# Kernel tuning notes

Hardware: AMD Instinct MI355X
Metric: run time of the kernel (lower is better)

The kernel has to match this reference:

```python
import jax, jax.numpy as jnp
import numpy as np

B, C, H, W = 8, 512, 64, 64
D = C // 8        # attention feature dim for q/k
HID = 100         # pooling hidden dim


def setup_inputs() -> dict:
    key = jax.random.key(0)
    ks = jax.random.split(key, 12)
    s = 0.02
    return {
        "x": jax.random.normal(ks[0], (B, C, H, W), dtype=jnp.float32),
        "Wq": jax.random.normal(ks[1], (D, C), dtype=jnp.float32) * s,
        "bq": jnp.zeros((D,), dtype=jnp.float32),
        "Wk": jax.random.normal(ks[2], (D, C), dtype=jnp.float32) * s,
        "bk": jnp.zeros((D,), dtype=jnp.float32),
        "Wv": jax.random.normal(ks[3], (C, C), dtype=jnp.float32) * s,
        "bv": jnp.zeros((C,), dtype=jnp.float32),
        "gamma": jnp.zeros((1,), dtype=jnp.float32),
        "Wa": jax.random.normal(ks[4], (HID, C), dtype=jnp.float32) * s,
        "ba": jnp.zeros((HID,), dtype=jnp.float32),
        "Wc": jax.random.normal(ks[5], (1, HID), dtype=jnp.float32) * s,
    }


def reference(x, Wq, bq, Wk, bk, Wv, bv, gamma, Wa, ba, Wc):
    b, c, h, w = x.shape
    n = h * w
    xf = x.reshape(b, c, n)  # [B, C, N]

    # 1x1 convs == per-pixel channel matmuls
    q = jnp.einsum('dc,bcn->bdn', Wq, xf) + bq[None, :, None]  # [B, D, N]
    k = jnp.einsum('dc,bcn->bdn', Wk, xf) + bk[None, :, None]  # [B, D, N]
    v = jnp.einsum('ec,bcn->ben', Wv, xf) + bv[None, :, None]  # [B, C, N]

    # energy[b,i,j] = <q_i, k_j>; softmax over j (last dim)
    energy = jnp.einsum('bdi,bdj->bij', q, k)                  # [B, N, N]
    attn = jax.nn.softmax(energy, axis=-1)
    # out[b,c,i] = sum_j v[b,c,j] * attn[b,i,j]
    sa_out = jnp.einsum('bcj,bij->bci', v, attn)               # [B, C, N]
    hfeat = gamma[0] * sa_out + xf                             # [B, C, N]

    # attention pooling: linear -> tanh -> linear -> softmax over spatial
    a = jnp.tanh(jnp.einsum('hc,bcn->bnh', Wa, hfeat) + ba)    # [B, N, HID]
    score = jnp.einsum('oh,bnh->bn', Wc, a)                    # [B, N]
    amap = jax.nn.softmax(score, axis=1)                       # [B, N]

    # weighted sum of ORIGINAL input features (as in the torch code)
    return jnp.einsum('bcn,bn->bc', xf, amap)                  # [B, C]
```

## Files before the change

### kernel.cpp

```cpp
#include <hip/hip_runtime.h>
#include <hip/hip_bf16.h>

#define B_ 8
#define C_ 512
#define N_ 4096
#define D_ 64
#define HID_ 100
#define LDK 40

typedef short bf16x8 __attribute__((ext_vector_type(8)));
typedef short bf16x4 __attribute__((ext_vector_type(4)));
typedef float f32x4 __attribute__((ext_vector_type(4)));

__device__ __forceinline__ short f2bf(float f) {
  unsigned u = __builtin_bit_cast(unsigned, f);
  u += 0x7fff + ((u >> 16) & 1);
  return (short)(u >> 16);
}

__device__ __forceinline__ float fast_tanh(float x) {
  float cx = fminf(fmaxf(x, -15.f), 15.f);
  float a = exp2f(cx * 2.885390082f);
  return (a - 1.f) * __builtin_amdgcn_rcpf(a + 1.f);
}


__global__ __launch_bounds__(256) void qkv_proj(
    const float* __restrict__ x,
    const float* __restrict__ Wq, const float* __restrict__ bq,
    const float* __restrict__ Wk, const float* __restrict__ bk,
    const float* __restrict__ Wv, const float* __restrict__ bv,
    const float* __restrict__ gamma,
    float* __restrict__ q, float* __restrict__ k, float* __restrict__ v) {
  if (gamma[0] == 0.0f) return;
  const int ROWS = D_ + D_ + C_;
  const int TILES = N_ / 256;
  const int NJOBS = B_ * ROWS * TILES;
  for (int job = blockIdx.x; job < NJOBS; job += gridDim.x) {
    int tile = job % TILES;
    int row  = (job / TILES) % ROWS;
    int b    = job / (TILES * ROWS);
    int n = tile * 256 + threadIdx.x;
    const float* W;
    float bias;
    float* dst;
    if (row < D_) {
      W = Wq + (size_t)row * C_; bias = bq[row];
      dst = q + ((size_t)b * D_ + row) * N_;
    } else if (row < 2 * D_) {
      int r = row - D_;
      W = Wk + (size_t)r * C_; bias = bk[r];
      dst = k + ((size_t)b * D_ + r) * N_;
    } else {
      int r = row - 2 * D_;
      W = Wv + (size_t)r * C_; bias = bv[r];
      dst = v + ((size_t)b * C_ + r) * N_;
    }
    const float* xb = x + (size_t)b * C_ * N_ + n;
    float s = 0.f;
    for (int c = 0; c < C_; ++c) s += W[c] * xb[(size_t)c * N_];
    dst[n] = s + bias;
  }
}

__global__ __launch_bounds__(256) void attn_sa(
    const float* __restrict__ q, const float* __restrict__ k,
    const float* __restrict__ v, const float* __restrict__ gamma,
    float* __restrict__ sa) {
  if (gamma[0] == 0.0f) return;
  __shared__ float e[N_];
  __shared__ float qi[D_];
  __shared__ float red4[4];
  const int tid = threadIdx.x;
  for (int job = blockIdx.x; job < B_ * N_; job += gridDim.x) {
    int b = job >> 12;
    int i = job & (N_ - 1);
    if (tid < D_) qi[tid] = q[((size_t)b * D_ + tid) * N_ + i];
    __syncthreads();
    for (int j = tid; j < N_; j += 256) {
      float s = 0.f;
      for (int d = 0; d < D_; ++d) s += qi[d] * k[((size_t)b * D_ + d) * N_ + j];
      e[j] = s;
    }
    __syncthreads();
    float m = -1e30f;
    for (int j = tid; j < N_; j += 256) m = fmaxf(m, e[j]);
#pragma unroll
    for (int off = 32; off; off >>= 1) m = fmaxf(m, __shfl_xor(m, off));
    if ((tid & 63) == 0) red4[tid >> 6] = m;
    __syncthreads();
    float M = fmaxf(fmaxf(red4[0], red4[1]), fmaxf(red4[2], red4[3]));
    __syncthreads();
    float ssum = 0.f;
    for (int j = tid; j < N_; j += 256) {
      float p = expf(e[j] - M);
      e[j] = p;
      ssum += p;
    }
#pragma unroll
    for (int off = 32; off; off >>= 1) ssum += __shfl_xor(ssum, off);
    if ((tid & 63) == 0) red4[tid >> 6] = ssum;
    __syncthreads();
    float inv = 1.0f / (red4[0] + red4[1] + red4[2] + red4[3]);
    __syncthreads();
    for (int c = tid; c < C_; c += 256) {
      const float* vr = v + ((size_t)b * C_ + c) * N_;
      float s = 0.f;
      for (int j = 0; j < N_; ++j) s += vr[j] * e[j];
      sa[((size_t)b * C_ + c) * N_ + i] = s * inv;
    }
    __syncthreads();
  }
}

__global__ __launch_bounds__(256) void wa_to_bf16(
    const float* __restrict__ Wa, short* __restrict__ wab) {
  int flat = (blockIdx.x * 256 + threadIdx.x) * 4;
  int h = flat >> 9, c = flat & 511;
  bf16x4 p = {0, 0, 0, 0};
  if (h < HID_) {
    float4 w4 = *(const float4*)&Wa[(size_t)h * C_ + c];
    p = (bf16x4){f2bf(w4.x), f2bf(w4.y), f2bf(w4.z), f2bf(w4.w)};
  }
  *(bf16x4*)&wab[flat] = p;
}


__global__ __launch_bounds__(512, 2) void pool_gemm(
    const float* __restrict__ x, const float* __restrict__ sa,
    const float* __restrict__ gamma,
    const short* __restrict__ wab, const float* __restrict__ ba,
    const float* __restrict__ Wc, float* __restrict__ score) {
  __shared__ short xls[2][256 * LDK];
  __shared__ float red[2][256];

  const int tid  = threadIdx.x;
  const int lane = tid & 63;
  const int w    = tid >> 6;
  const int wn   = w & 3;
  const int wh   = w >> 2;
  const int r16  = lane & 15;
  const int gq   = lane >> 4;
  const int b    = blockIdx.x >> 4;
  const int n0   = (blockIdx.x & 15) * 256;
  const float g  = gamma[0];

  const int mn = tid & 63;
  const int mc = tid >> 6;
  const float* xb  = x  + (size_t)b * C_ * N_ + n0 + 4 * mn;
  const float* sab = sa + (size_t)b * C_ * N_ + n0 + 4 * mn;

  const short* wpr = wab + (size_t)(wh * 64 + r16) * C_ + 8 * gq;

  f32x4 acc[4][4];
#pragma unroll
  for (int i = 0; i < 4; ++i)
#pragma unroll
    for (int f = 0; f < 4; ++f) acc[i][f] = (f32x4){0.f, 0.f, 0.f, 0.f};

  float4 ra[3][4];
  bf16x8 bc[4], bn[4];

#define LOAD_T(slot, t)                                                      \
  do {                                                                       \
    _Pragma("unroll")                                                        \
    for (int r = 0; r < 4; ++r)                                              \
      ra[slot][r] = *(const float4*)&xb[(size_t)((t) * 32 + 4 * mc + r) * N_]; \
  } while (0)

#define WRITE_T(buf, slot, t)                                                \
  do {                                                                       \
    if (g != 0.0f) {                                                         \
      _Pragma("unroll")                                                      \
      for (int r = 0; r < 4; ++r) {                                          \
        float4 s4 = *(const float4*)&sab[(size_t)((t) * 32 + 4 * mc + r) * N_]; \
        ra[slot][r].x += g * s4.x; ra[slot][r].y += g * s4.y;                \
        ra[slot][r].z += g * s4.z; ra[slot][r].w += g * s4.w;                \
      }                                                                      \
    }                                                                        \
    _Pragma("unroll")                                                        \
    for (int j = 0; j < 4; ++j) {                                            \
      float v0 = (j == 0) ? ra[slot][0].x : (j == 1) ? ra[slot][0].y         \
               : (j == 2) ? ra[slot][0].z : ra[slot][0].w;                   \
      float v1 = (j == 0) ? ra[slot][1].x : (j == 1) ? ra[slot][1].y         \
               : (j == 2) ? ra[slot][1].z : ra[slot][1].w;                   \
      float v2 = (j == 0) ? ra[slot][2].x : (j == 1) ? ra[slot][2].y         \
               : (j == 2) ? ra[slot][2].z : ra[slot][2].w;                   \
      float v3 = (j == 0) ? ra[slot][3].x : (j == 1) ? ra[slot][3].y         \
               : (j == 2) ? ra[slot][3].z : ra[slot][3].w;                   \
      bf16x4 pk = {f2bf(v0), f2bf(v1), f2bf(v2), f2bf(v3)};                  \
      *(bf16x4*)&xls[buf][(4 * mn + j) * LDK + 4 * mc] = pk;                 \
    }                                                                        \
  } while (0)

#define BLOAD(dst, cc)                                                       \
  do {                                                                       \
    _Pragma("unroll")                                                        \
    for (int f = 0; f < 4; ++f)                                              \
      dst[f] = *(const bf16x8*)&wpr[(size_t)f * 16 * C_ + (cc) * 32];        \
  } while (0)

  LOAD_T(0, 0);
  LOAD_T(1, 1);
  BLOAD(bc, 0);
  WRITE_T(0, 0, 0);
  __syncthreads();

#pragma unroll
  for (int t = 0; t < 16; ++t) {
    if (t + 2 < 16) LOAD_T((t + 2) % 3, t + 2);
    BLOAD(bn, (t + 1) & 15);
#pragma unroll
    for (int nf = 0; nf < 4; ++nf) {
      bf16x8 af = *(const bf16x8*)
          &xls[t & 1][(wn * 64 + nf * 16 + r16) * LDK + 8 * gq];
#pragma unroll
      for (int f = 0; f < 4; ++f)
        acc[nf][f] =
            __builtin_amdgcn_mfma_f32_16x16x32_bf16(af, bc[f], acc[nf][f], 0, 0, 0);
    }
    if (t + 1 < 16) WRITE_T((t + 1) & 1, (t + 1) % 3, t + 1);
#pragma unroll
    for (int f = 0; f < 4; ++f) bc[f] = bn[f];
    __syncthreads();
  }

  float wcv[4], bav[4];
#pragma unroll
  for (int f = 0; f < 4; ++f) {
    int h = (wh * 4 + f) * 16 + r16;
    wcv[f] = (h < HID_) ? Wc[h] : 0.f;
    bav[f] = (h < HID_) ? ba[h] : 0.f;
  }
  float p[16];
#pragma unroll
  for (int nf = 0; nf < 4; ++nf) {
#pragma unroll
    for (int j = 0; j < 4; ++j) {
      float s = 0.f;
#pragma unroll
      for (int f = 0; f < 4; ++f)
        s += wcv[f] * fast_tanh(acc[nf][f][j] + bav[f]);
      p[nf * 4 + j] = s;
    }
  }
#pragma unroll
  for (int off = 1; off < 16; off <<= 1) {
#pragma unroll
    for (int i = 0; i < 16; ++i) p[i] += __shfl_xor(p[i], off);
  }
  float keep = p[0];
#pragma unroll
  for (int i = 1; i < 16; ++i)
    if (r16 == i) keep = p[i];
  red[wh][wn * 64 + (r16 >> 2) * 16 + gq * 4 + (r16 & 3)] = keep;
  __syncthreads();
  if (tid < 256)
    score[(size_t)b * N_ + n0 + tid] = red[0][tid] + red[1][tid];
}

__global__ __launch_bounds__(256) void softmax_n(
    const float* __restrict__ score, float* __restrict__ amap) {
  const int b = blockIdx.x;
  const int tid = threadIdx.x;
  __shared__ float red4[4];
  float m = -1e30f;
  for (int i = tid; i < N_; i += 256) m = fmaxf(m, score[(size_t)b * N_ + i]);
#pragma unroll
  for (int off = 32; off; off >>= 1) m = fmaxf(m, __shfl_xor(m, off));
  if ((tid & 63) == 0) red4[tid >> 6] = m;
  __syncthreads();
  float M = fmaxf(fmaxf(red4[0], red4[1]), fmaxf(red4[2], red4[3]));
  __syncthreads();
  float s = 0.f;
  for (int i = tid; i < N_; i += 256) s += expf(score[(size_t)b * N_ + i] - M);
#pragma unroll
  for (int off = 32; off; off >>= 1) s += __shfl_xor(s, off);
  if ((tid & 63) == 0) red4[tid >> 6] = s;
  __syncthreads();
  float inv = 1.0f / (red4[0] + red4[1] + red4[2] + red4[3]);
  for (int i = tid; i < N_; i += 256)
    amap[(size_t)b * N_ + i] = expf(score[(size_t)b * N_ + i] - M) * inv;
}

__global__ __launch_bounds__(256) void wsum_kernel(
    const float* __restrict__ x, const float* __restrict__ amap,
    float* __restrict__ out) {
  const int b = blockIdx.x >> 9;
  const int c = blockIdx.x & 511;
  const float4* xr = (const float4*)(x + ((size_t)b * C_ + c) * N_);
  const float4* am = (const float4*)(amap + (size_t)b * N_);
  float s = 0.f;
  for (int i = threadIdx.x; i < N_ / 4; i += 256) {
    float4 xv = xr[i];
    float4 av = am[i];
    s += xv.x * av.x + xv.y * av.y + xv.z * av.z + xv.w * av.w;
  }
#pragma unroll
  for (int off = 32; off; off >>= 1) s += __shfl_xor(s, off);
  __shared__ float red4[4];
  if ((threadIdx.x & 63) == 0) red4[threadIdx.x >> 6] = s;
  __syncthreads();
  if (threadIdx.x == 0)
    out[blockIdx.x] = red4[0] + red4[1] + red4[2] + red4[3];
}

extern "C" void kernel_launch(void* const* d_in, const int* in_sizes, int n_in,
                              void* d_out, int out_size, void* d_ws, size_t ws_size,
                              hipStream_t stream) {
  const float* x     = (const float*)d_in[0];
  const float* Wq    = (const float*)d_in[1];
  const float* bq    = (const float*)d_in[2];
  const float* Wk    = (const float*)d_in[3];
  const float* bk    = (const float*)d_in[4];
  const float* Wv    = (const float*)d_in[5];
  const float* bv    = (const float*)d_in[6];
  const float* gamma = (const float*)d_in[7];
  const float* Wa    = (const float*)d_in[8];
  const float* ba    = (const float*)d_in[9];
  const float* Wc    = (const float*)d_in[10];
  float* out = (float*)d_out;

  float* ws    = (float*)d_ws;
  float* score = ws;
  float* amap  = ws + 32768;
  short* wab   = (short*)(ws + 65536);
  float* q  = ws + 65536 + 40960;
  float* k  = q + (size_t)B_ * D_ * N_;
  float* v  = k + (size_t)B_ * D_ * N_;
  float* sa = v + (size_t)B_ * C_ * N_;

  wa_to_bf16<<<64, 256, 0, stream>>>(Wa, wab);
  qkv_proj<<<256, 256, 0, stream>>>(x, Wq, bq, Wk, bk, Wv, bv, gamma, q, k, v);
  attn_sa<<<256, 256, 0, stream>>>(q, k, v, gamma, sa);
  pool_gemm<<<B_ * (N_ / 256), 512, 0, stream>>>(x, sa, gamma, wab, ba, Wc, score);
  softmax_n<<<B_, 256, 0, stream>>>(score, amap);
  wsum_kernel<<<B_ * C_, 256, 0, stream>>>(x, amap, out);
}
```

Before: 58.80 us.

## Retile pool_gemm to 64-pixel blocks with wider channel steps and more blocks

The pooling GEMM now gives each block 64 pixels instead of 256, so there are 512 blocks instead of 128. Each K-step covers 128 channels, split into four 32-wide LDS sub-tiles, and B fragments are read straight from global memory inside the compute loop. The launch bound now targets 4 blocks per CU, which cuts register use (fewer accumulators, one load slot instead of triple buffering). The goal is to fill more CUs and improve occupancy for this memory-bound pass over x. The cost is more Wa weight reloads per block and a shallower prefetch pipeline.

```diff
diff --git a/kernel.cpp b/kernel.cpp
--- a/kernel.cpp
+++ b/kernel.cpp
@@ -126,13 +126,13 @@
 }
 
 
-__global__ __launch_bounds__(512, 2) void pool_gemm(
+__global__ __launch_bounds__(512, 4) void pool_gemm(
     const float* __restrict__ x, const float* __restrict__ sa,
     const float* __restrict__ gamma,
     const short* __restrict__ wab, const float* __restrict__ ba,
     const float* __restrict__ Wc, float* __restrict__ score) {
-  __shared__ short xls[2][256 * LDK];
-  __shared__ float red[2][256];
+  __shared__ short xls[2][4][64 * LDK];
+  __shared__ float red[2][64];
 
   const int tid  = threadIdx.x;
   const int lane = tid & 63;
@@ -141,87 +141,72 @@
   const int wh   = w >> 2;
   const int r16  = lane & 15;
   const int gq   = lane >> 4;
-  const int b    = blockIdx.x >> 4;
-  const int n0   = (blockIdx.x & 15) * 256;
+  const int b    = blockIdx.x >> 6;
+  const int n0   = (blockIdx.x & 63) * 64;
   const float g  = gamma[0];
 
-  const int mn = tid & 63;
-  const int mc = tid >> 6;
+  const int mn = tid & 15;
+  const int mc = tid >> 4;
   const float* xb  = x  + (size_t)b * C_ * N_ + n0 + 4 * mn;
   const float* sab = sa + (size_t)b * C_ * N_ + n0 + 4 * mn;
 
   const short* wpr = wab + (size_t)(wh * 64 + r16) * C_ + 8 * gq;
 
-  f32x4 acc[4][4];
-#pragma unroll
-  for (int i = 0; i < 4; ++i)
-#pragma unroll
-    for (int f = 0; f < 4; ++f) acc[i][f] = (f32x4){0.f, 0.f, 0.f, 0.f};
-
-  float4 ra[3][4];
-  bf16x8 bc[4], bn[4];
-
-#define LOAD_T(slot, t)                                                      \
+  f32x4 acc[4];
+#pragma unroll
+  for (int f = 0; f < 4; ++f) acc[f] = (f32x4){0.f, 0.f, 0.f, 0.f};
+
+  f32x4 ra[4];
+
+#define LOAD_T(t)                                                            \
   do {                                                                       \
     _Pragma("unroll")                                                        \
     for (int r = 0; r < 4; ++r)                                              \
-      ra[slot][r] = *(const float4*)&xb[(size_t)((t) * 32 + 4 * mc + r) * N_]; \
+      ra[r] = *(const f32x4*)&xb[(size_t)((t) * 128 + 4 * mc + r) * N_];     \
   } while (0)
 
-#define WRITE_T(buf, slot, t)                                                \
+#define WRITE_T(buf, t)                                                      \
   do {                                                                       \
     if (g != 0.0f) {                                                         \
       _Pragma("unroll")                                                      \
       for (int r = 0; r < 4; ++r) {                                          \
-        float4 s4 = *(const float4*)&sab[(size_t)((t) * 32 + 4 * mc + r) * N_]; \
-        ra[slot][r].x += g * s4.x; ra[slot][r].y += g * s4.y;                \
-        ra[slot][r].z += g * s4.z; ra[slot][r].w += g * s4.w;                \
+        f32x4 s4 = *(const f32x4*)&sab[(size_t)((t) * 128 + 4 * mc + r) * N_]; \
+        ra[r] += g * s4;                                                     \
       }                                                                      \
     }                                                                        \
     _Pragma("unroll")                                                        \
     for (int j = 0; j < 4; ++j) {                                            \
-      float v0 = (j == 0) ? ra[slot][0].x : (j == 1) ? ra[slot][0].y         \
-               : (j == 2) ? ra[slot][0].z : ra[slot][0].w;                   \
-      float v1 = (j == 0) ? ra[slot][1].x : (j == 1) ? ra[slot][1].y         \
-               : (j == 2) ? ra[slot][1].z : ra[slot][1].w;                   \
-      float v2 = (j == 0) ? ra[slot][2].x : (j == 1) ? ra[slot][2].y         \
-               : (j == 2) ? ra[slot][2].z : ra[slot][2].w;                   \
-      float v3 = (j == 0) ? ra[slot][3].x : (j == 1) ? ra[slot][3].y         \
-               : (j == 2) ? ra[slot][3].z : ra[slot][3].w;                   \
-      bf16x4 pk = {f2bf(v0), f2bf(v1), f2bf(v2), f2bf(v3)};                  \
-      *(bf16x4*)&xls[buf][(4 * mn + j) * LDK + 4 * mc] = pk;                 \
+      bf16x4 pk = {f2bf(ra[0][j]), f2bf(ra[1][j]), f2bf(ra[2][j]),           \
+                   f2bf(ra[3][j])};                                          \
+      *(bf16x4*)&xls[buf][mc >> 3][(4 * mn + j) * LDK + (mc & 7) * 4] = pk;  \
     }                                                                        \
   } while (0)
 
-#define BLOAD(dst, cc)                                                       \
+#define COMPUTE(buf, t)                                                      \
   do {                                                                       \
     _Pragma("unroll")                                                        \
-    for (int f = 0; f < 4; ++f)                                              \
-      dst[f] = *(const bf16x8*)&wpr[(size_t)f * 16 * C_ + (cc) * 32];        \
+    for (int s = 0; s < 4; ++s) {                                            \
+      bf16x8 af =                                                            \
+          *(const bf16x8*)&xls[buf][s][(wn * 16 + r16) * LDK + 8 * gq];      \
+      _Pragma("unroll")                                                      \
+      for (int f = 0; f < 4; ++f) {                                          \
+        bf16x8 bfr = *(const bf16x8*)                                        \
+            &wpr[(size_t)(f * 16) * C_ + (t) * 128 + s * 32];                \
+        acc[f] =                                                             \
+            __builtin_amdgcn_mfma_f32_16x16x32_bf16(af, bfr, acc[f], 0, 0, 0); \
+      }                                                                      \
+    }                                                                        \
   } while (0)
 
-  LOAD_T(0, 0);
-  LOAD_T(1, 1);
-  BLOAD(bc, 0);
-  WRITE_T(0, 0, 0);
-  __syncthreads();
-
-#pragma unroll
-  for (int t = 0; t < 16; ++t) {
-    if (t + 2 < 16) LOAD_T((t + 2) % 3, t + 2);
-    BLOAD(bn, (t + 1) & 15);
-#pragma unroll
-    for (int nf = 0; nf < 4; ++nf) {
-      bf16x8 af = *(const bf16x8*)
-          &xls[t & 1][(wn * 64 + nf * 16 + r16) * LDK + 8 * gq];
-#pragma unroll
-      for (int f = 0; f < 4; ++f)
-        acc[nf][f] =
-            __builtin_amdgcn_mfma_f32_16x16x32_bf16(af, bc[f], acc[nf][f], 0, 0, 0);
-    }
-    if (t + 1 < 16) WRITE_T((t + 1) & 1, (t + 1) % 3, t + 1);
-#pragma unroll
-    for (int f = 0; f < 4; ++f) bc[f] = bn[f];
+  LOAD_T(0);
+  WRITE_T(0, 0);
+  __syncthreads();
+
+#pragma unroll
+  for (int t = 0; t < 4; ++t) {
+    if (t < 3) LOAD_T(t + 1);
+    COMPUTE(t & 1, t);
+    if (t < 3) WRITE_T((t + 1) & 1, t + 1);
     __syncthreads();
   }
 
@@ -232,30 +217,22 @@
     wcv[f] = (h < HID_) ? Wc[h] : 0.f;
     bav[f] = (h < HID_) ? ba[h] : 0.f;
   }
-  float p[16];
-#pragma unroll
-  for (int nf = 0; nf < 4; ++nf) {
-#pragma unroll
-    for (int j = 0; j < 4; ++j) {
-      float s = 0.f;
-#pragma unroll
-      for (int f = 0; f < 4; ++f)
-        s += wcv[f] * fast_tanh(acc[nf][f][j] + bav[f]);
-      p[nf * 4 + j] = s;
-    }
+  f32x4 part = {0.f, 0.f, 0.f, 0.f};
+#pragma unroll
+  for (int f = 0; f < 4; ++f) {
+#pragma unroll
+    for (int j = 0; j < 4; ++j)
+      part[j] += wcv[f] * fast_tanh(acc[f][j] + bav[f]);
   }
 #pragma unroll
   for (int off = 1; off < 16; off <<= 1) {
 #pragma unroll
-    for (int i = 0; i < 16; ++i) p[i] += __shfl_xor(p[i], off);
-  }
-  float keep = p[0];
-#pragma unroll
-  for (int i = 1; i < 16; ++i)
-    if (r16 == i) keep = p[i];
-  red[wh][wn * 64 + (r16 >> 2) * 16 + gq * 4 + (r16 & 3)] = keep;
-  __syncthreads();
-  if (tid < 256)
+    for (int j = 0; j < 4; ++j) part[j] += __shfl_xor(part[j], off);
+  }
+  if (r16 == 0)
+    *(f32x4*)&red[wh][wn * 16 + gq * 4] = part;
+  __syncthreads();
+  if (tid < 64)
     score[(size_t)b * N_ + n0 + tid] = red[0][tid] + red[1][tid];
 }
 
@@ -333,7 +310,7 @@
   wa_to_bf16<<<64, 256, 0, stream>>>(Wa, wab);
   qkv_proj<<<256, 256, 0, stream>>>(x, Wq, bq, Wk, bk, Wv, bv, gamma, q, k, v);
   attn_sa<<<256, 256, 0, stream>>>(q, k, v, gamma, sa);
-  pool_gemm<<<B_ * (N_ / 256), 512, 0, stream>>>(x, sa, gamma, wab, ba, Wc, score);
+  pool_gemm<<<B_ * (N_ / 64), 512, 0, stream>>>(x, sa, gamma, wab, ba, Wc, score);
   softmax_n<<<B_, 256, 0, stream>>>(score, amap);
   wsum_kernel<<<B_ * C_, 256, 0, stream>>>(x, amap, out);
 }
```

Measured after the change: 68.95 us. 1.17x slower.
